# Kernel optimization log

Hardware: AMD Instinct MI355X
Metric: run time of the kernel (lower is better)

The kernel has to match this reference:

```python
import jax, jax.numpy as jnp
import numpy as np

NEG_SLOPE = 0.2  # PyG GATConv LeakyReLU slope


def _gat_conv(x, ei, W, a_src, a_dst, bias, concat):
    # x: [N, F_in], ei: [2, E] (with self-loops), W: [F_in, H*C], a_*: [H, C]
    N = x.shape[0]
    H, C = a_src.shape
    xp = (x @ W).reshape(N, H, C)                       # [N, H, C]
    src, dst = ei[0], ei[1]
    s_score = jnp.einsum('nhc,hc->nh', xp, a_src)       # [N, H]
    d_score = jnp.einsum('nhc,hc->nh', xp, a_dst)       # [N, H]
    e = jax.nn.leaky_relu(s_score[src] + d_score[dst], negative_slope=NEG_SLOPE)  # [E, H]
    # segment softmax over incoming edges of each dst node
    m = jax.ops.segment_max(e, dst, num_segments=N)     # [N, H]
    ex = jnp.exp(e - m[dst])                            # [E, H]
    den = jax.ops.segment_sum(ex, dst, num_segments=N)  # [N, H]
    alpha = ex / den[dst]                               # [E, H]
    msg = alpha[:, :, None] * xp[src]                   # [E, H, C]
    out = jax.ops.segment_sum(msg, dst, num_segments=N) # [N, H, C]
    out = out.reshape(N, H * C) if concat else out.mean(axis=1)
    return out + bias


def _add_self_loops(edge_index, num_nodes):
    ar = jnp.arange(num_nodes, dtype=edge_index.dtype)
    return jnp.concatenate([edge_index, jnp.stack([ar, ar])], axis=1)


def setup_inputs() -> dict:
    key = jax.random.key(0)
    ks = jax.random.split(key, 16)
    N, E, F_in, Hd, heads, out_c, G = 50000, 800000, 128, 64, 4, 10, 64
    x = jax.random.normal(ks[0], (N, F_in), dtype=jnp.float32)
    edge_index = jax.random.randint(ks[1], (2, E), 0, N, dtype=jnp.int64)
    batch = jnp.sort(jax.random.randint(ks[2], (N,), 0, G, dtype=jnp.int64))
    sc = lambda f: 1.0 / np.sqrt(f)
    # layer 1: in -> hidden, heads=4, concat
    W1 = jax.random.normal(ks[3], (F_in, heads * Hd), dtype=jnp.float32) * sc(F_in)
    a_src1 = jax.random.normal(ks[4], (heads, Hd), dtype=jnp.float32) * sc(Hd)
    a_dst1 = jax.random.normal(ks[5], (heads, Hd), dtype=jnp.float32) * sc(Hd)
    b1 = jnp.zeros((heads * Hd,), dtype=jnp.float32)
    # layer 2: heads*hidden -> hidden, heads=1, concat=False
    W2 = jax.random.normal(ks[6], (heads * Hd, Hd), dtype=jnp.float32) * sc(heads * Hd)
    a_src2 = jax.random.normal(ks[7], (1, Hd), dtype=jnp.float32) * sc(Hd)
    a_dst2 = jax.random.normal(ks[8], (1, Hd), dtype=jnp.float32) * sc(Hd)
    b2 = jnp.zeros((Hd,), dtype=jnp.float32)
    # final linear
    Wl = jax.random.normal(ks[9], (Hd, out_c), dtype=jnp.float32) * sc(Hd)
    bl = jnp.zeros((out_c,), dtype=jnp.float32)
    return {"x": x, "edge_index": edge_index, "batch": batch,
            "W1": W1, "a_src1": a_src1, "a_dst1": a_dst1, "b1": b1,
            "W2": W2, "a_src2": a_src2, "a_dst2": a_dst2, "b2": b2,
            "Wl": Wl, "bl": bl}


def reference(x, edge_index, batch, W1, a_src1, a_dst1, b1,
              W2, a_src2, a_dst2, b2, Wl, bl):
    N = x.shape[0]
    G = 64  # number of graphs
    ei = _add_self_loops(edge_index, N)
    h = jax.nn.elu(_gat_conv(x, ei, W1, a_src1, a_dst1, b1, concat=True))
    h = jax.nn.elu(_gat_conv(h, ei, W2, a_src2, a_dst2, b2, concat=False))
    # global mean pool over graphs
    sums = jax.ops.segment_sum(h, batch, num_segments=G)            # [G, Hd]
    cnt = jax.ops.segment_sum(jnp.ones((N,), h.dtype), batch, num_segments=G)
    pooled = sums / jnp.maximum(cnt, 1.0)[:, None]
    return pooled @ Wl + bl
```

## Files before the change

### kernel.cpp

```cpp
#include <hip/hip_runtime.h>
#include <hip/hip_bf16.h>
#include <cstdint>

#define NN   50000
#define NE   800000
#define NET  850000
#define FIN  128
#define FH1  256
#define HD   64
#define NG   64
#define OUTC 10
#define NBS  ((NN + 255) / 256)

typedef __attribute__((ext_vector_type(8))) short short8v;
typedef __attribute__((ext_vector_type(4))) float f32x4;

__device__ __forceinline__ float bf2f(unsigned short u) {
    union { unsigned int i; float f; } v; v.i = ((unsigned int)u) << 16; return v.f;
}
__device__ __forceinline__ float bflo(unsigned int u) {
    union { unsigned int i; float f; } v; v.i = u << 16; return v.f;
}
__device__ __forceinline__ float bfhi(unsigned int u) {
    union { unsigned int i; float f; } v; v.i = u & 0xFFFF0000u; return v.f;
}
__device__ __forceinline__ unsigned short f2bf(float f) {
    union { float fl; unsigned int i; } v; v.fl = f;
    unsigned int x = v.i;
    return (unsigned short)((x + 0x7FFFu + ((x >> 16) & 1u)) >> 16);
}
__device__ __forceinline__ float leakyr(float v) { return v > 0.f ? v : 0.2f * v; }
__device__ __forceinline__ float elu1(float v)  { return v > 0.f ? v : expm1f(v); }

__global__ __launch_bounds__(256) void k_gemm1(
    const float* __restrict__ x, const float* __restrict__ W1,
    const float* __restrict__ asrc, const float* __restrict__ adst,
    unsigned short* __restrict__ xp1, float* __restrict__ s1t, float* __restrict__ d1)
{
    __shared__ __align__(16) short Ash[64 * 40];
    __shared__ __align__(16) short Bsh[256 * 40];
    int row0 = blockIdx.x * 64;
    int tid  = threadIdx.x;
    int wv   = tid >> 6;
    int lane = tid & 63;
    int g    = lane >> 4;
    int c    = lane & 15;

    f32x4 acc[4][4];
    #pragma unroll
    for (int i = 0; i < 4; i++)
        #pragma unroll
        for (int j = 0; j < 4; j++) acc[i][j] = (f32x4){0.f, 0.f, 0.f, 0.f};

    int sr = tid >> 2;
    int sq = tid & 3;

    for (int k0 = 0; k0 < FIN; k0 += 32) {
        {
            int gr = row0 + sr;
            float4 v0 = make_float4(0,0,0,0), v1 = make_float4(0,0,0,0);
            if (gr < NN) {
                const float4* p = reinterpret_cast<const float4*>(x + (size_t)gr * FIN + k0 + sq * 8);
                v0 = p[0]; v1 = p[1];
            }
            short8v pk;
            pk[0] = (short)f2bf(v0.x); pk[1] = (short)f2bf(v0.y);
            pk[2] = (short)f2bf(v0.z); pk[3] = (short)f2bf(v0.w);
            pk[4] = (short)f2bf(v1.x); pk[5] = (short)f2bf(v1.y);
            pk[6] = (short)f2bf(v1.z); pk[7] = (short)f2bf(v1.w);
            *reinterpret_cast<short8v*>(&Ash[sr * 40 + sq * 8]) = pk;
        }
        {
            #pragma unroll
            for (int kg = 0; kg < 4; kg++) {
                short8v pk;
                #pragma unroll
                for (int i = 0; i < 8; i++)
                    pk[i] = (short)f2bf(W1[(size_t)(k0 + kg * 8 + i) * FH1 + tid]);
                *reinterpret_cast<short8v*>(&Bsh[tid * 40 + kg * 8]) = pk;
            }
        }
        __syncthreads();
        short8v bf[4];
        #pragma unroll
        for (int j = 0; j < 4; j++)
            bf[j] = *reinterpret_cast<const short8v*>(&Bsh[(64 * wv + 16 * j + c) * 40 + g * 8]);
        #pragma unroll
        for (int rt = 0; rt < 4; rt++) {
            short8v af = *reinterpret_cast<const short8v*>(&Ash[(16 * rt + c) * 40 + g * 8]);
            #pragma unroll
            for (int j = 0; j < 4; j++)
                acc[rt][j] = __builtin_amdgcn_mfma_f32_16x16x32_bf16(af, bf[j], acc[rt][j], 0, 0, 0);
        }
        __syncthreads();
    }

    float as[4], ad[4];
    #pragma unroll
    for (int j = 0; j < 4; j++) {
        as[j] = asrc[64 * wv + 16 * j + c];
        ad[j] = adst[64 * wv + 16 * j + c];
    }
    #pragma unroll
    for (int rt = 0; rt < 4; rt++) {
        #pragma unroll
        for (int r = 0; r < 4; r++) {
            int row = row0 + 16 * rt + 4 * g + r;
            float sv = 0.f, dv = 0.f;
            #pragma unroll
            for (int j = 0; j < 4; j++) {
                float v = acc[rt][j][r];
                sv = fmaf(v, as[j], sv);
                dv = fmaf(v, ad[j], dv);
                if (row < NN) xp1[((size_t)wv * NN + row) * HD + 16 * j + c] = f2bf(v);
            }
            #pragma unroll
            for (int off = 8; off >= 1; off >>= 1) {
                sv += __shfl_xor(sv, off, 16);
                dv += __shfl_xor(dv, off, 16);
            }
            if (c == 0 && row < NN) {
                s1t[(size_t)wv * NN + row] = sv;
                d1[row * 4 + wv] = dv;
            }
        }
    }
}

__global__ __launch_bounds__(256) void k_hist(
    const int* __restrict__ ei, int* __restrict__ deg)
{
    int e = blockIdx.x * 256 + threadIdx.x;
    if (e >= NET) return;
    int dst = (e < NE) ? ei[NE + e] : (e - NE);
    atomicAdd(&deg[dst], 1);
}

__global__ __launch_bounds__(256) void k_scan_a(
    const int* __restrict__ deg, int* __restrict__ part)
{
    __shared__ int sm[256];
    int t = threadIdx.x;
    int idx = blockIdx.x * 256 + t;
    sm[t] = (idx < NN) ? deg[idx] : 0;
    __syncthreads();
    for (int off = 128; off >= 1; off >>= 1) {
        if (t < off) sm[t] += sm[t + off];
        __syncthreads();
    }
    if (t == 0) part[blockIdx.x] = sm[0];
}

__global__ __launch_bounds__(256) void k_scan_b(
    int* __restrict__ part, int* __restrict__ rowptr)
{
    __shared__ int sm[256];
    int t = threadIdx.x;
    int v = (t < NBS) ? part[t] : 0;
    sm[t] = v;
    __syncthreads();
    for (int off = 1; off < 256; off <<= 1) {
        int u = (t >= off) ? sm[t - off] : 0;
        __syncthreads();
        sm[t] += u;
        __syncthreads();
    }
    if (t < NBS) part[t] = sm[t] - v;
    if (t == 0) rowptr[NN] = NET;
}

__global__ __launch_bounds__(256) void k_scan_c(
    const int* __restrict__ deg, const int* __restrict__ part,
    int* __restrict__ rowptr)
{
    __shared__ int sm[256];
    int t = threadIdx.x;
    int idx = blockIdx.x * 256 + t;
    int v = (idx < NN) ? deg[idx] : 0;
    sm[t] = v;
    __syncthreads();
    for (int off = 1; off < 256; off <<= 1) {
        int u = (t >= off) ? sm[t - off] : 0;
        __syncthreads();
        sm[t] += u;
        __syncthreads();
    }
    if (idx < NN) rowptr[idx] = part[blockIdx.x] + sm[t] - v;
}

__global__ __launch_bounds__(256) void k_scatter(
    const int* __restrict__ ei, const int* __restrict__ rowptr,
    int* __restrict__ cursor, int* __restrict__ eidx)
{
    int e = blockIdx.x * 256 + threadIdx.x;
    if (e >= NET) return;
    int src, dst;
    if (e < NE) { src = ei[e]; dst = ei[NE + e]; }
    else        { src = dst = e - NE; }
    int pos = atomicAdd(&cursor[dst], 1);
    eidx[rowptr[dst] + pos] = src;
}

__global__ __launch_bounds__(256) void k_pull1(
    const int* __restrict__ rowptr, const int* __restrict__ eidx,
    const float* __restrict__ s1t, const float* __restrict__ d1,
    const unsigned short* __restrict__ xp1, const float* __restrict__ b1,
    unsigned short* __restrict__ h1)
{
    int b = blockIdx.x;
    int head = (b >> 1) & 3;
    int ng = ((b >> 3) << 1) | (b & 1);
    int wv = threadIdx.x >> 6;
    int lane = threadIdx.x & 63;
    int n = ng * 4 + wv;
    if (n >= NN) return;
    const float* sh = s1t + (size_t)head * NN;
    const unsigned short* xph = xp1 + (size_t)head * NN * HD;
    float dv = d1[(size_t)n * 4 + head];
    int jb = __builtin_amdgcn_readfirstlane(rowptr[n]);
    int je = __builtin_amdgcn_readfirstlane(rowptr[n + 1]);
    float a = 0.f, den = 0.f;
    int j = jb;
    for (; j + 8 <= je; j += 8) {
        int s[8];
        #pragma unroll
        for (int q = 0; q < 8; q++) s[q] = eidx[j + q];
        float sc[8];
        unsigned short xv[8];
        #pragma unroll
        for (int q = 0; q < 8; q++) {
            sc[q] = sh[s[q]];
            xv[q] = xph[(size_t)s[q] * HD + lane];
        }
        #pragma unroll
        for (int q = 0; q < 8; q++) {
            float ex = __expf(leakyr(sc[q] + dv));
            a = fmaf(bf2f(xv[q]), ex, a);
            den += ex;
        }
    }
    for (; j < je; j++) {
        int src = eidx[j];
        float ex = __expf(leakyr(sh[src] + dv));
        a = fmaf(bf2f(xph[(size_t)src * HD + lane]), ex, a);
        den += ex;
    }
    float o = elu1(a / den + b1[head * HD + lane]);
    h1[(size_t)n * FH1 + head * HD + lane] = f2bf(o);
}

__global__ __launch_bounds__(256) void k_gemm2(
    const unsigned short* __restrict__ h1, const float* __restrict__ W2,
    const float* __restrict__ asrc2, const float* __restrict__ adst2,
    unsigned short* __restrict__ xp2, float* __restrict__ s2, float* __restrict__ d2)
{
    __shared__ __align__(16) short Ash[64 * 40];
    __shared__ __align__(16) short Bsh[64 * 40];
    int row0 = blockIdx.x * 64;
    int tid  = threadIdx.x;
    int wv   = tid >> 6;
    int lane = tid & 63;
    int g    = lane >> 4;
    int c    = lane & 15;

    f32x4 acc[4] = {{0,0,0,0},{0,0,0,0},{0,0,0,0},{0,0,0,0}};

    int sr = tid >> 2;
    int sq = tid & 3;

    for (int k0 = 0; k0 < FH1; k0 += 32) {
        {
            int gr = row0 + sr;
            uint4 v = make_uint4(0, 0, 0, 0);
            if (gr < NN) v = *reinterpret_cast<const uint4*>(h1 + (size_t)gr * FH1 + k0 + sq * 8);
            *reinterpret_cast<uint4*>(&Ash[sr * 40 + sq * 8]) = v;
        }
        {
            int n  = tid & 63;
            int kg = tid >> 6;
            short8v pk;
            #pragma unroll
            for (int i = 0; i < 8; i++)
                pk[i] = (short)f2bf(W2[(size_t)(k0 + kg * 8 + i) * HD + n]);
            *reinterpret_cast<short8v*>(&Bsh[n * 40 + kg * 8]) = pk;
        }
        __syncthreads();
        short8v af = *reinterpret_cast<const short8v*>(&Ash[(16 * wv + c) * 40 + g * 8]);
        #pragma unroll
        for (int j = 0; j < 4; j++) {
            short8v bf = *reinterpret_cast<const short8v*>(&Bsh[(16 * j + c) * 40 + g * 8]);
            acc[j] = __builtin_amdgcn_mfma_f32_16x16x32_bf16(af, bf, acc[j], 0, 0, 0);
        }
        __syncthreads();
    }

    float as[4], ad[4];
    #pragma unroll
    for (int j = 0; j < 4; j++) {
        as[j] = asrc2[16 * j + c];
        ad[j] = adst2[16 * j + c];
    }
    #pragma unroll
    for (int r = 0; r < 4; r++) {
        int row = row0 + 16 * wv + 4 * g + r;
        float sv = 0.f, dv = 0.f;
        #pragma unroll
        for (int j = 0; j < 4; j++) {
            float v = acc[j][r];
            sv = fmaf(v, as[j], sv);
            dv = fmaf(v, ad[j], dv);
            if (row < NN) xp2[(size_t)row * HD + 16 * j + c] = f2bf(v);
        }
        #pragma unroll
        for (int off = 8; off >= 1; off >>= 1) {
            sv += __shfl_xor(sv, off, 16);
            dv += __shfl_xor(dv, off, 16);
        }
        if (c == 0 && row < NN) { s2[row] = sv; d2[row] = dv; }
    }
}

__global__ __launch_bounds__(256) void k_pull2(
    const int* __restrict__ rowptr, const int* __restrict__ eidx,
    const float* __restrict__ s2, const float* __restrict__ d2,
    const unsigned short* __restrict__ xp2, const float* __restrict__ b2,
    float* __restrict__ h2)
{
    int wv = threadIdx.x >> 6;
    int lane = threadIdx.x & 63;
    int n = blockIdx.x * 4 + wv;
    if (n >= NN) return;
    int half = lane >> 5;
    int c = lane & 31;
    float dv = d2[n];
    int jb = __builtin_amdgcn_readfirstlane(rowptr[n]);
    int je = __builtin_amdgcn_readfirstlane(rowptr[n + 1]);
    float a0 = 0.f, a1 = 0.f, den = 0.f;
    int j = jb;
    for (; j + 16 <= je; j += 16) {
        #pragma unroll
        for (int p = 0; p < 8; p++) {
            int e = j + 2 * p + half;
            int src = eidx[e];
            float sc = s2[src];
            unsigned int u = *reinterpret_cast<const unsigned int*>(xp2 + (size_t)src * HD + 2 * c);
            float ex = __expf(leakyr(sc + dv));
            a0 = fmaf(bflo(u), ex, a0);
            a1 = fmaf(bfhi(u), ex, a1);
            den += ex;
        }
    }
    for (; j < je; j += 2) {
        int e = j + half;
        bool valid = e < je;
        int ec = valid ? e : (je - 1);
        int src = eidx[ec];
        float sc = s2[src];
        unsigned int u = *reinterpret_cast<const unsigned int*>(xp2 + (size_t)src * HD + 2 * c);
        float ex = valid ? __expf(leakyr(sc + dv)) : 0.f;
        a0 = fmaf(bflo(u), ex, a0);
        a1 = fmaf(bfhi(u), ex, a1);
        den += ex;
    }
    a0 += __shfl_xor(a0, 32);
    a1 += __shfl_xor(a1, 32);
    den += __shfl_xor(den, 32);
    if (half == 0) {
        float inv = 1.0f / den;
        float2 bb = *reinterpret_cast<const float2*>(b2 + 2 * c);
        float2 o;
        o.x = elu1(fmaf(a0, inv, bb.x));
        o.y = elu1(fmaf(a1, inv, bb.y));
        *reinterpret_cast<float2*>(h2 + (size_t)n * HD + 2 * c) = o;
    }
}

__global__ __launch_bounds__(256) void k_pool(
    const float* __restrict__ h2, const int* __restrict__ batch,
    float* __restrict__ pooled )
{
    int g = blockIdx.x;
    int sslice = blockIdx.y;
    int lo = 0, hi = NN;
    while (lo < hi) { int m = (lo + hi) >> 1; if (batch[m] < g) lo = m + 1; else hi = m; }
    int start = lo;
    hi = NN;
    while (lo < hi) { int m = (lo + hi) >> 1; if (batch[m] < g + 1) lo = m + 1; else hi = m; }
    int end = lo;
    int len = end - start;
    int chunk = (len + 7) >> 3;
    int b0 = start + sslice * chunk;
    int b1 = min(b0 + chunk, end);
    int c = threadIdx.x & 63;
    int rg = threadIdx.x >> 6;
    float sum = 0.f;
    for (int n = b0 + rg; n < b1; n += 4)
        sum += h2[(size_t)n * HD + c];
    __shared__ float red[4][64];
    red[rg][c] = sum;
    __syncthreads();
    if (threadIdx.x < 64) {
        float tot = red[0][c] + red[1][c] + red[2][c] + red[3][c];
        if (tot != 0.f) atomicAdd(&pooled[g * HD + c], tot);
    }
}

__global__ __launch_bounds__(256) void k_final(
    const float* __restrict__ pooled, const int* __restrict__ batch,
    const float* __restrict__ Wl, const float* __restrict__ bl,
    float* __restrict__ out)
{
    int t = blockIdx.x * 256 + threadIdx.x;
    if (t >= NG * OUTC) return;
    int g = t / OUTC, o = t % OUTC;
    int lo = 0, hi = NN;
    while (lo < hi) { int m = (lo + hi) >> 1; if (batch[m] < g) lo = m + 1; else hi = m; }
    int start = lo;
    hi = NN;
    while (lo < hi) { int m = (lo + hi) >> 1; if (batch[m] < g + 1) lo = m + 1; else hi = m; }
    float cnt = (float)(lo - start);
    float acc = 0.f;
    #pragma unroll
    for (int k = 0; k < HD; k++)
        acc = fmaf(pooled[g * HD + k], Wl[k * OUTC + o], acc);
    out[t] = acc / fmaxf(cnt, 1.f) + bl[o];
}

extern "C" void kernel_launch(void* const* d_in, const int* in_sizes, int n_in,
                              void* d_out, int out_size, void* d_ws, size_t ws_size,
                              hipStream_t stream) {
    const float* x     = (const float*)d_in[0];
    const int*   ei    = (const int*)d_in[1];
    const int*   batch = (const int*)d_in[2];
    const float* W1    = (const float*)d_in[3];
    const float* as1   = (const float*)d_in[4];
    const float* ad1   = (const float*)d_in[5];
    const float* b1    = (const float*)d_in[6];
    const float* W2    = (const float*)d_in[7];
    const float* as2   = (const float*)d_in[8];
    const float* ad2   = (const float*)d_in[9];
    const float* b2    = (const float*)d_in[10];
    const float* Wl    = (const float*)d_in[11];
    const float* bl    = (const float*)d_in[12];
    float* out = (float*)d_out;

    char* w = (char*)d_ws;
    size_t off = 0;
    auto alloc = [&](size_t bytes) {
        void* p = (void*)(w + off);
        off = (off + bytes + 255) & ~(size_t)255;
        return p;
    };
    int* deg    = (int*)alloc((size_t)NN * 4);
    int* cursor = (int*)alloc((size_t)NN * 4);
    float* pooled = (float*)alloc((size_t)NG * HD * 4);
    size_t zbytes = off;
    int* part   = (int*)alloc((size_t)NBS * 4);
    int* rowptr = (int*)alloc((size_t)(NN + 1) * 4);
    int* eidx   = (int*)alloc((size_t)NET * 4);
    unsigned short* xp1 = (unsigned short*)alloc((size_t)NN * FH1 * 2);
    unsigned short* h1  = (unsigned short*)alloc((size_t)NN * FH1 * 2);
    float* s1t = (float*)alloc((size_t)NN * 4 * 4);
    float* d1s = (float*)alloc((size_t)NN * 4 * 4);
    unsigned short* xp2 = (unsigned short*)alloc((size_t)NN * HD * 2);
    float* s2  = (float*)alloc((size_t)NN * 4);
    float* d2s = (float*)alloc((size_t)NN * 4);
    float* h2  = (float*)alloc((size_t)NN * HD * 4);

    hipMemsetAsync(d_ws, 0, zbytes, stream);

    k_hist   <<<(NET + 255) / 256, 256, 0, stream>>>(ei, deg);
    k_scan_a <<<NBS, 256, 0, stream>>>(deg, part);
    k_scan_b <<<1, 256, 0, stream>>>(part, rowptr);
    k_scan_c <<<NBS, 256, 0, stream>>>(deg, part, rowptr);
    k_scatter<<<(NET + 255) / 256, 256, 0, stream>>>(ei, rowptr, cursor, eidx);

    k_gemm1<<<(NN + 63) / 64, 256, 0, stream>>>(x, W1, as1, ad1, xp1, s1t, d1s);
    k_pull1<<<NN, 256, 0, stream>>>(rowptr, eidx, s1t, d1s, xp1, b1, h1);
    k_gemm2<<<(NN + 63) / 64, 256, 0, stream>>>(h1, W2, as2, ad2, xp2, s2, d2s);
    k_pull2<<<(NN + 3) / 4, 256, 0, stream>>>(rowptr, eidx, s2, d2s, xp2, b2, h2);
    dim3 gp(NG, 8);
    k_pool <<<gp, 256, 0, stream>>>(h2, batch, pooled);
    k_final<<<(NG * OUTC + 255) / 256, 256, 0, stream>>>(pooled, batch, Wl, bl, out);
}
```

Before: 309.7 us.

## Precompute layer-1 edge attention exponentials in CSR order during scatter

Moves k_gemm1 ahead of the CSR build so k_scatter can compute exp(leakyrelu(s[src]+d[dst])) for all four heads and store them per head in CSR edge order. k_pull1 then reads these values contiguously instead of gathering s scores at random src indices and evaluating exp per edge per lane. In exchange, scatter writes an extra 13.6 MB edge array with scattered stores, and the s1 layout becomes node-major so four heads can be read with one float4 load.

```diff
diff --git a/kernel.cpp b/kernel.cpp
--- a/kernel.cpp
+++ b/kernel.cpp
@@ -35,7 +35,7 @@
 __global__ __launch_bounds__(256) void k_gemm1(
     const float* __restrict__ x, const float* __restrict__ W1,
     const float* __restrict__ asrc, const float* __restrict__ adst,
-    unsigned short* __restrict__ xp1, float* __restrict__ s1t, float* __restrict__ d1)
+    unsigned short* __restrict__ xp1, float* __restrict__ s1, float* __restrict__ d1)
 {
     __shared__ __align__(16) short Ash[64 * 40];
     __shared__ __align__(16) short Bsh[256 * 40];
@@ -120,7 +120,7 @@
                 dv += __shfl_xor(dv, off, 16);
             }
             if (c == 0 && row < NN) {
-                s1t[(size_t)wv * NN + row] = sv;
+                s1[row * 4 + wv] = sv;
                 d1[row * 4 + wv] = dv;
             }
         }
@@ -190,7 +190,9 @@
 
 __global__ __launch_bounds__(256) void k_scatter(
     const int* __restrict__ ei, const int* __restrict__ rowptr,
-    int* __restrict__ cursor, int* __restrict__ eidx)
+    int* __restrict__ cursor, int* __restrict__ eidx,
+    const float* __restrict__ s1, const float* __restrict__ d1,
+    float* __restrict__ es1t)
 {
     int e = blockIdx.x * 256 + threadIdx.x;
     if (e >= NET) return;
@@ -198,12 +200,19 @@
     if (e < NE) { src = ei[e]; dst = ei[NE + e]; }
     else        { src = dst = e - NE; }
     int pos = atomicAdd(&cursor[dst], 1);
-    eidx[rowptr[dst] + pos] = src;
+    int p = rowptr[dst] + pos;
+    eidx[p] = src;
+    float4 s = *reinterpret_cast<const float4*>(s1 + (size_t)src * 4);
+    float4 d = *reinterpret_cast<const float4*>(d1 + (size_t)dst * 4);
+    es1t[0 * NET + p] = __expf(leakyr(s.x + d.x));
+    es1t[1 * NET + p] = __expf(leakyr(s.y + d.y));
+    es1t[2 * NET + p] = __expf(leakyr(s.z + d.z));
+    es1t[3 * NET + p] = __expf(leakyr(s.w + d.w));
 }
 
 __global__ __launch_bounds__(256) void k_pull1(
     const int* __restrict__ rowptr, const int* __restrict__ eidx,
-    const float* __restrict__ s1t, const float* __restrict__ d1,
+    const float* __restrict__ es1t,
     const unsigned short* __restrict__ xp1, const float* __restrict__ b1,
     unsigned short* __restrict__ h1)
 {
@@ -214,35 +223,34 @@
     int lane = threadIdx.x & 63;
     int n = ng * 4 + wv;
     if (n >= NN) return;
-    const float* sh = s1t + (size_t)head * NN;
     const unsigned short* xph = xp1 + (size_t)head * NN * HD;
-    float dv = d1[(size_t)n * 4 + head];
+    const float* esh = es1t + (size_t)head * NET;
     int jb = __builtin_amdgcn_readfirstlane(rowptr[n]);
     int je = __builtin_amdgcn_readfirstlane(rowptr[n + 1]);
     float a = 0.f, den = 0.f;
     int j = jb;
     for (; j + 8 <= je; j += 8) {
         int s[8];
-        #pragma unroll
-        for (int q = 0; q < 8; q++) s[q] = eidx[j + q];
-        float sc[8];
+        float es[8];
+        #pragma unroll
+        for (int q = 0; q < 8; q++) {
+            s[q] = eidx[j + q];
+            es[q] = esh[j + q];
+        }
         unsigned short xv[8];
         #pragma unroll
+        for (int q = 0; q < 8; q++)
+            xv[q] = xph[(size_t)s[q] * HD + lane];
+        #pragma unroll
         for (int q = 0; q < 8; q++) {
-            sc[q] = sh[s[q]];
-            xv[q] = xph[(size_t)s[q] * HD + lane];
-        }
-        #pragma unroll
-        for (int q = 0; q < 8; q++) {
-            float ex = __expf(leakyr(sc[q] + dv));
-            a = fmaf(bf2f(xv[q]), ex, a);
-            den += ex;
+            a = fmaf(bf2f(xv[q]), es[q], a);
+            den += es[q];
         }
     }
     for (; j < je; j++) {
-        int src = eidx[j];
-        float ex = __expf(leakyr(sh[src] + dv));
-        a = fmaf(bf2f(xph[(size_t)src * HD + lane]), ex, a);
+        int s = eidx[j];
+        float ex = esh[j];
+        a = fmaf(bf2f(xph[(size_t)s * HD + lane]), ex, a);
         den += ex;
     }
     float o = elu1(a / den + b1[head * HD + lane]);
@@ -458,9 +466,10 @@
     int* part   = (int*)alloc((size_t)NBS * 4);
     int* rowptr = (int*)alloc((size_t)(NN + 1) * 4);
     int* eidx   = (int*)alloc((size_t)NET * 4);
+    float* es1t = (float*)alloc((size_t)NET * 4 * 4);
     unsigned short* xp1 = (unsigned short*)alloc((size_t)NN * FH1 * 2);
     unsigned short* h1  = (unsigned short*)alloc((size_t)NN * FH1 * 2);
-    float* s1t = (float*)alloc((size_t)NN * 4 * 4);
+    float* s1  = (float*)alloc((size_t)NN * 4 * 4);
     float* d1s = (float*)alloc((size_t)NN * 4 * 4);
     unsigned short* xp2 = (unsigned short*)alloc((size_t)NN * HD * 2);
     float* s2  = (float*)alloc((size_t)NN * 4);
@@ -469,14 +478,14 @@
 
     hipMemsetAsync(d_ws, 0, zbytes, stream);
 
+    k_gemm1<<<(NN + 63) / 64, 256, 0, stream>>>(x, W1, as1, ad1, xp1, s1, d1s);
     k_hist   <<<(NET + 255) / 256, 256, 0, stream>>>(ei, deg);
     k_scan_a <<<NBS, 256, 0, stream>>>(deg, part);
     k_scan_b <<<1, 256, 0, stream>>>(part, rowptr);
     k_scan_c <<<NBS, 256, 0, stream>>>(deg, part, rowptr);
-    k_scatter<<<(NET + 255) / 256, 256, 0, stream>>>(ei, rowptr, cursor, eidx);
-
-    k_gemm1<<<(NN + 63) / 64, 256, 0, stream>>>(x, W1, as1, ad1, xp1, s1t, d1s);
-    k_pull1<<<NN, 256, 0, stream>>>(rowptr, eidx, s1t, d1s, xp1, b1, h1);
+    k_scatter<<<(NET + 255) / 256, 256, 0, stream>>>(ei, rowptr, cursor, eidx, s1, d1s, es1t);
+
+    k_pull1<<<NN, 256, 0, stream>>>(rowptr, eidx, es1t, xp1, b1, h1);
     k_gemm2<<<(NN + 63) / 64, 256, 0, stream>>>(h1, W2, as2, ad2, xp2, s2, d2s);
     k_pull2<<<(NN + 3) / 4, 256, 0, stream>>>(rowptr, eidx, s2, d2s, xp2, b2, h2);
     dim3 gp(NG, 8);
```

After: 319.4 us. 3.2% more time.
